# Kernel optimization log

Measured on AMD Instinct MI355X. Metric: run time of the kernel, lower is better.

## Reference

```python
import jax, jax.numpy as jnp
import numpy as np

N_NODES = 100_000
N_EDGES = 1_600_000
IN_DIM = 500
HID = 128
OUT = 16
DEG = 3          # Chebyshev 'order' -> DEG+1 basis terms
N_KAN_USED = 2   # forward applies kan_layers[:num_layers-1] with num_layers=3


def spmm(edge_index, h):
    # torch.sparse.mm(A, h) with A = COO(edge_index, ones, (N, N)):
    # out[row] = sum over edges of h[col]
    return jax.ops.segment_sum(h[edge_index[1]], edge_index[0], num_segments=N_NODES)


def cheb_kan(h, coeffs):
    # ChebyKANLayer: t = tanh(h); basis T_k(t) = cos(k*arccos(t)) computed via
    # the (mathematically identical, numerically stable) recurrence.
    t = jnp.tanh(h)                                  # [N, HID]
    Ts = [jnp.ones_like(t), t]
    for _ in range(DEG - 1):
        Ts.append(2.0 * t * Ts[-1] - Ts[-2])
    basis = jnp.stack(Ts, axis=-1)                   # [N, HID, DEG+1]
    return jnp.einsum('nid,iod->no', basis, coeffs)  # [N, HID]


def setup_inputs() -> dict:
    key = jax.random.key(0)
    ks = jax.random.split(key, 6)
    x = jax.random.normal(ks[0], (N_NODES, IN_DIM), dtype=jnp.float32)
    edge_index = jax.random.randint(ks[1], (2, N_EDGES), 0, N_NODES)
    W_in = jax.random.normal(ks[2], (IN_DIM, HID), dtype=jnp.float32) / np.sqrt(IN_DIM)
    cheb_coeffs = jax.random.normal(ks[3], (N_KAN_USED, HID, HID, DEG + 1),
                                    dtype=jnp.float32) / (HID * (DEG + 1))
    W_out = jax.random.normal(ks[4], (HID, OUT), dtype=jnp.float32) / np.sqrt(HID)
    return {"x": x, "edge_index": edge_index, "W_in": W_in,
            "cheb_coeffs": cheb_coeffs, "W_out": W_out}


def reference(x, edge_index, W_in, cheb_coeffs, W_out):
    h = x @ W_in                      # linear_input (no bias)
    # dropout is identity at inference
    h = spmm(edge_index, h)           # sparse adjacency aggregation
    for l in range(N_KAN_USED):
        h = cheb_kan(h, cheb_coeffs[l])
        h = spmm(edge_index, h)
    logits = h @ W_out                # output_layer (no bias)
    return jax.nn.log_softmax(logits, axis=-1)
```

## Files before the change

kernel.cpp:

```cpp
#include <hip/hip_runtime.h>
#include <hip/hip_bf16.h>

#define N_NODES 100000
#define N_EDGES 1600000
#define IN_DIM  500
#define HID     128
#define KDIM    512
#define NB      782
#define BCAP    4096

#define NG_GEMM 1563
#define NG_BIN  6250

typedef __attribute__((ext_vector_type(8))) short bf16x8;
typedef __attribute__((ext_vector_type(4))) float f32x4;

__device__ inline short f2bf(float x) {
    union { float f; unsigned u; } v; v.f = x;
    unsigned r = (v.u + 0x7FFFu + ((v.u >> 16) & 1u)) >> 16;
    return (short)r;
}
__device__ inline float bf_lo(unsigned u) { union { unsigned u; float f; } v; v.u = u << 16; return v.f; }
__device__ inline float bf_hi(unsigned u) { union { unsigned u; float f; } v; v.u = u & 0xFFFF0000u; return v.f; }

__device__ inline bf16x8 cheb_frag(unsigned v) {
    float hx[2] = {bf_lo(v), bf_hi(v)};
    short t[8];
#pragma unroll
    for (int q = 0; q < 2; q++) {
        float xx = fminf(fmaxf(hx[q], -15.f), 15.f);
        float e  = __expf(2.f * xx);
        float tt = (e - 1.f) / (e + 1.f);
        float T2 = 2.f * tt * tt - 1.f;
        float T3 = 2.f * tt * T2 - tt;
        t[q * 4 + 0] = (short)0x3F80;
        t[q * 4 + 1] = f2bf(tt);
        t[q * 4 + 2] = f2bf(T2);
        t[q * 4 + 3] = f2bf(T3);
    }
    return *(bf16x8*)&t[0];
}

__global__ __launch_bounds__(256) void repack_all(const float* __restrict__ cheb,
                                                  const float* __restrict__ W,
                                                  const float* __restrict__ Wout,
                                                  unsigned short* __restrict__ Bmat,
                                                  unsigned short* __restrict__ Wmat,
                                                  unsigned short* __restrict__ C2W) {
    const int b = blockIdx.x;
    if (b < 256) {
        int idx = b * 256 + threadIdx.x;
        int o = idx >> 9;
        int k = idx & 511;
        int i = k >> 2;
        int d = k & 3;
        Bmat[idx] = (unsigned short)f2bf(cheb[i * 512 + o * 4 + d]);
    } else if (b < 512) {
        int idx = (b - 256) * 256 + threadIdx.x;
        int o = idx >> 9;
        int k = idx & 511;
        Wmat[idx] = (k < IN_DIM) ? (unsigned short)f2bf(W[k * HID + o]) : 0;
    } else {
        int idx = (b - 512) * 256 + threadIdx.x;
        int o16 = idx >> 9;
        int k   = idx & 511;
        const float* cb = cheb + 65536 + (k >> 2) * 512 + (k & 3);
        float s = 0.f;
#pragma unroll 4
        for (int o = 0; o < 128; o++) s += cb[o * 4] * Wout[o * 16 + o16];
        C2W[o16 * 512 + k] = (unsigned short)f2bf(s);
    }
}

__global__ __launch_bounds__(256, 4) void prep_kernel(const float* __restrict__ x,
                                                      const int* __restrict__ ei,
                                                      const unsigned short* __restrict__ Wmat,
                                                      unsigned short* __restrict__ hA,
                                                      int* __restrict__ bcnt,
                                                      unsigned* __restrict__ bbuf) {
    __shared__ __align__(16) short Bs[2][128][40];
    const int tid = threadIdx.x;

    if (blockIdx.x < NG_GEMM) {
        const int lane = tid & 63;
        const int wave = tid >> 6;
        const int quad = lane >> 4;
        const int l16  = lane & 15;
        const int n0   = blockIdx.x * 64;
        const int br   = tid >> 1;
        const int bh   = tid & 1;

        int row = n0 + wave * 16 + l16; if (row >= N_NODES) row = N_NODES - 1;
        const float* __restrict__ xrow = x + (long)row * IN_DIM;

        f32x4 acc[8];
#pragma unroll
        for (int nt = 0; nt < 8; nt++)
#pragma unroll
            for (int r = 0; r < 4; r++) acc[nt][r] = 0.f;

        auto loadA = [&](int kt, float (&v)[8]) {
            const int kb = kt * 32 + quad * 8;
            if (kb + 8 <= IN_DIM) {
                const float4* s4 = (const float4*)(xrow + kb);
                float4 a0 = s4[0], a1 = s4[1];
                v[0]=a0.x; v[1]=a0.y; v[2]=a0.z; v[3]=a0.w;
                v[4]=a1.x; v[5]=a1.y; v[6]=a1.z; v[7]=a1.w;
            } else {
#pragma unroll
                for (int q = 0; q < 8; q++) v[q] = (kb + q < IN_DIM) ? xrow[kb + q] : 0.f;
            }
        };
        auto loadB = [&](int kt, bf16x8 (&w)[2]) {
            w[0] = *(const bf16x8*)&Wmat[br * 512 + kt * 32 + bh * 16];
            w[1] = *(const bf16x8*)&Wmat[br * 512 + kt * 32 + bh * 16 + 8];
        };
        auto storeB = [&](int buf, const bf16x8 (&w)[2]) {
            *(bf16x8*)&Bs[buf][br][bh * 16]     = w[0];
            *(bf16x8*)&Bs[buf][br][bh * 16 + 8] = w[1];
        };
        auto mfmaTile = [&](int buf, const float (&v)[8]) {
            short t[8];
#pragma unroll
            for (int q = 0; q < 8; q++) t[q] = f2bf(v[q]);
            bf16x8 a = *(bf16x8*)&t[0];
#pragma unroll
            for (int nt = 0; nt < 8; nt++) {
                bf16x8 b = *(const bf16x8*)&Bs[buf][nt * 16 + l16][quad * 8];
                acc[nt] = __builtin_amdgcn_mfma_f32_16x16x32_bf16(a, b, acc[nt], 0, 0, 0);
            }
        };

        float  va[8], vb[8];
        bf16x8 wa[2], wb[2];
        loadA(0, va); loadB(0, wa);
        for (int kt = 0; kt < 16; kt += 2) {
            storeB(0, wa);
            loadB(kt + 1, wb);
            loadA(kt + 1, vb);
            __syncthreads();
            mfmaTile(0, va);
            storeB(1, wb);
            if (kt + 2 < 16) { loadB(kt + 2, wa); loadA(kt + 2, va); }
            __syncthreads();
            mfmaTile(1, vb);
        }

        int mrow = n0 + wave * 16 + quad * 4;
#pragma unroll
        for (int r = 0; r < 4; r++) {
            int n = mrow + r;
            if (n < N_NODES) {
#pragma unroll
                for (int nt = 0; nt < 8; nt++)
                    hA[(long)n * HID + nt * 16 + l16] = (unsigned short)f2bf(acc[nt][r]);
            }
        }
    } else {
        int e = (blockIdx.x - NG_GEMM) * 256 + tid;
        if (e < N_EDGES) {
            int r = ei[e];
            int c = ei[N_EDGES + e];
            int b = r >> 7;
            int p = atomicAdd(&bcnt[b * 16], 1);
            if (p < BCAP) bbuf[b * BCAP + p] = ((unsigned)(r & 127) << 17) | (unsigned)c;
        }
    }
}

__global__ __launch_bounds__(256) void place_kernel(const unsigned* __restrict__ buf,
                                                    const int* __restrict__ bcnt,
                                                    int* __restrict__ gctr,
                                                    int* __restrict__ row_start,
                                                    int* __restrict__ row_cnt,
                                                    int* __restrict__ col_sorted) {
    __shared__ int hist[128];
    __shared__ int scan[128];
    __shared__ int cur[128];
    __shared__ int base_s;
    const int b = blockIdx.x, tid = threadIdx.x;
    int cnt = bcnt[b * 16]; if (cnt > BCAP) cnt = BCAP;
    if (tid < 128) hist[tid] = 0;
    __syncthreads();
    for (int i = tid; i < cnt; i += 256)
        atomicAdd(&hist[buf[b * BCAP + i] >> 17], 1);
    __syncthreads();
    if (tid < 128) scan[tid] = hist[tid];
    __syncthreads();
    for (int off = 1; off < 128; off <<= 1) {
        int t = (tid < 128 && tid >= off) ? scan[tid - off] : 0;
        __syncthreads();
        if (tid < 128) scan[tid] += t;
        __syncthreads();
    }
    if (tid == 0) base_s = atomicAdd(gctr, scan[127]);
    __syncthreads();
    const int base = base_s;
    if (tid < 128) {
        int excl = scan[tid] - hist[tid] + base;
        cur[tid] = excl;
        int r = b * 128 + tid;
        if (r < N_NODES) { row_start[r] = excl; row_cnt[r] = hist[tid]; }
    }
    __syncthreads();
    for (int i = tid; i < cnt; i += 256) {
        unsigned u = buf[b * BCAP + i];
        int rl = (int)(u >> 17);
        int c  = (int)(u & 0x1FFFFu);
        int pos = atomicAdd(&cur[rl], 1);
        col_sorted[pos] = c;
    }
}

__global__ __launch_bounds__(256, 4) void cheb_gemm(const unsigned short* __restrict__ h,
                                                    const unsigned short* __restrict__ Bmat,
                                                    unsigned short* __restrict__ out) {
    __shared__ __align__(16) short Bs[2][128][40];
    const int tid  = threadIdx.x;
    const int lane = tid & 63;
    const int wave = tid >> 6;
    const int quad = lane >> 4;
    const int l16  = lane & 15;
    const int n0   = blockIdx.x * 64;
    const int br   = tid >> 1;
    const int bh   = tid & 1;

    int row = n0 + wave * 16 + l16; if (row >= N_NODES) row = N_NODES - 1;
    const unsigned short* __restrict__ hrow = h + (long)row * HID;

    unsigned hreg[16];
#pragma unroll
    for (int kt = 0; kt < 16; kt++)
        hreg[kt] = *(const unsigned*)(hrow + kt * 8 + quad * 2);

    f32x4 acc[8];
#pragma unroll
    for (int nt = 0; nt < 8; nt++)
#pragma unroll
        for (int r = 0; r < 4; r++) acc[nt][r] = 0.f;

    auto loadB = [&](int kt, bf16x8 (&w)[2]) {
        w[0] = *(const bf16x8*)&Bmat[br * 512 + kt * 32 + bh * 16];
        w[1] = *(const bf16x8*)&Bmat[br * 512 + kt * 32 + bh * 16 + 8];
    };
    auto storeB = [&](int buf, const bf16x8 (&w)[2]) {
        *(bf16x8*)&Bs[buf][br][bh * 16]     = w[0];
        *(bf16x8*)&Bs[buf][br][bh * 16 + 8] = w[1];
    };
    auto mfmaTile = [&](int buf, int kt) {
        bf16x8 a = cheb_frag(hreg[kt]);
#pragma unroll
        for (int nt = 0; nt < 8; nt++) {
            bf16x8 b = *(const bf16x8*)&Bs[buf][nt * 16 + l16][quad * 8];
            acc[nt] = __builtin_amdgcn_mfma_f32_16x16x32_bf16(a, b, acc[nt], 0, 0, 0);
        }
    };

    bf16x8 wa[2], wb[2];
    loadB(0, wa);
    for (int kt = 0; kt < 16; kt += 2) {
        storeB(0, wa);
        loadB(kt + 1, wb);
        __syncthreads();
        mfmaTile(0, kt);
        storeB(1, wb);
        if (kt + 2 < 16) loadB(kt + 2, wa);
        __syncthreads();
        mfmaTile(1, kt + 1);
    }

    {
        int mrow = n0 + wave * 16 + quad * 4;
#pragma unroll
        for (int r = 0; r < 4; r++) {
            int n = mrow + r;
            if (n < N_NODES) {
#pragma unroll
                for (int nt = 0; nt < 8; nt++)
                    out[(long)n * HID + nt * 16 + l16] = (unsigned short)f2bf(acc[nt][r]);
            }
        }
    }
}

__global__ __launch_bounds__(256, 4) void cheb16_gemm(const unsigned short* __restrict__ h,
                                                      const unsigned short* __restrict__ C2W,
                                                      float* __restrict__ z) {
    __shared__ __align__(16) short Bs16[16][520];
    const int tid  = threadIdx.x;
    const int lane = tid & 63;
    const int wave = tid >> 6;
    const int quad = lane >> 4;
    const int l16  = lane & 15;
    const int n0   = blockIdx.x * 64;

    {
        int o16 = tid >> 4;
        int seg = tid & 15;
        *(bf16x8*)&Bs16[o16][seg * 32]      = *(const bf16x8*)&C2W[o16 * 512 + seg * 32];
        *(bf16x8*)&Bs16[o16][seg * 32 + 8]  = *(const bf16x8*)&C2W[o16 * 512 + seg * 32 + 8];
        *(bf16x8*)&Bs16[o16][seg * 32 + 16] = *(const bf16x8*)&C2W[o16 * 512 + seg * 32 + 16];
        *(bf16x8*)&Bs16[o16][seg * 32 + 24] = *(const bf16x8*)&C2W[o16 * 512 + seg * 32 + 24];
    }

    int row = n0 + wave * 16 + l16; if (row >= N_NODES) row = N_NODES - 1;
    const unsigned short* __restrict__ hrow = h + (long)row * HID;

    unsigned hreg[16];
#pragma unroll
    for (int kt = 0; kt < 16; kt++)
        hreg[kt] = *(const unsigned*)(hrow + kt * 8 + quad * 2);

    f32x4 acc;
#pragma unroll
    for (int r = 0; r < 4; r++) acc[r] = 0.f;

    __syncthreads();

#pragma unroll
    for (int kt = 0; kt < 16; kt++) {
        bf16x8 a = cheb_frag(hreg[kt]);
        bf16x8 b = *(const bf16x8*)&Bs16[l16][kt * 32 + quad * 8];
        acc = __builtin_amdgcn_mfma_f32_16x16x32_bf16(a, b, acc, 0, 0, 0);
    }

    {
        int mrow = n0 + wave * 16 + quad * 4;
#pragma unroll
        for (int r = 0; r < 4; r++) {
            int n = mrow + r;
            if (n < N_NODES) z[n * 16 + l16] = acc[r];
        }
    }
}

__global__ __launch_bounds__(256) void spmm_gather(const int* __restrict__ row_start,
                                                   const int* __restrict__ row_cnt,
                                                   const int* __restrict__ col_sorted,
                                                   const unsigned short* __restrict__ h,
                                                   unsigned short* __restrict__ out) {
    const int wid  = (blockIdx.x * 256 + threadIdx.x) >> 6;
    const int lane = threadIdx.x & 63;
    const int sub  = lane >> 4;
    const int fl   = lane & 15;
    if (wid >= N_NODES) return;
    const int s = row_start[wid];
    const int e = s + row_cnt[wid];
    const uint4* __restrict__ h4 = (const uint4*)h;

    float a[8], b[8];
#pragma unroll
    for (int q = 0; q < 8; q++) { a[q] = 0.f; b[q] = 0.f; }

    int j = s;
    for (; j + 8 <= e; j += 8) {
        int c0 = col_sorted[j + sub];
        int c1 = col_sorted[j + 4 + sub];
        uint4 u0 = h4[c0 * 16 + fl];
        uint4 u1 = h4[c1 * 16 + fl];
        a[0] += bf_lo(u0.x); a[1] += bf_hi(u0.x);
        a[2] += bf_lo(u0.y); a[3] += bf_hi(u0.y);
        a[4] += bf_lo(u0.z); a[5] += bf_hi(u0.z);
        a[6] += bf_lo(u0.w); a[7] += bf_hi(u0.w);
        b[0] += bf_lo(u1.x); b[1] += bf_hi(u1.x);
        b[2] += bf_lo(u1.y); b[3] += bf_hi(u1.y);
        b[4] += bf_lo(u1.z); b[5] += bf_hi(u1.z);
        b[6] += bf_lo(u1.w); b[7] += bf_hi(u1.w);
    }
    for (; j < e; j += 4) {
        int idx = j + sub;
        float m = (idx < e) ? 1.f : 0.f;
        int ci = (idx < e) ? idx : (e - 1);
        int c = col_sorted[ci];
        uint4 u = h4[c * 16 + fl];
        a[0] = fmaf(m, bf_lo(u.x), a[0]); a[1] = fmaf(m, bf_hi(u.x), a[1]);
        a[2] = fmaf(m, bf_lo(u.y), a[2]); a[3] = fmaf(m, bf_hi(u.y), a[3]);
        a[4] = fmaf(m, bf_lo(u.z), a[4]); a[5] = fmaf(m, bf_hi(u.z), a[5]);
        a[6] = fmaf(m, bf_lo(u.w), a[6]); a[7] = fmaf(m, bf_hi(u.w), a[7]);
    }
#pragma unroll
    for (int q = 0; q < 8; q++) a[q] += b[q];
#pragma unroll
    for (int q = 0; q < 8; q++) {
        a[q] += __shfl_xor(a[q], 16);
        a[q] += __shfl_xor(a[q], 32);
    }
    if (sub == 0) {
        unsigned w0 = (unsigned)(unsigned short)f2bf(a[0]) | ((unsigned)(unsigned short)f2bf(a[1]) << 16);
        unsigned w1 = (unsigned)(unsigned short)f2bf(a[2]) | ((unsigned)(unsigned short)f2bf(a[3]) << 16);
        unsigned w2 = (unsigned)(unsigned short)f2bf(a[4]) | ((unsigned)(unsigned short)f2bf(a[5]) << 16);
        unsigned w3 = (unsigned)(unsigned short)f2bf(a[6]) | ((unsigned)(unsigned short)f2bf(a[7]) << 16);
        uint4 pw; pw.x = w0; pw.y = w1; pw.z = w2; pw.w = w3;
        ((uint4*)out)[wid * 16 + fl] = pw;
    }
}

__global__ __launch_bounds__(256) void spmm_out(const int* __restrict__ row_start,
                                                const int* __restrict__ row_cnt,
                                                const int* __restrict__ col_sorted,
                                                const float* __restrict__ z,
                                                float* __restrict__ out) {
    const int wid  = (blockIdx.x * 256 + threadIdx.x) >> 6;
    const int lane = threadIdx.x & 63;
    const int sub  = lane >> 4;
    const int fl   = lane & 15;
    if (wid >= N_NODES) return;
    const int s = row_start[wid];
    const int e = s + row_cnt[wid];

    float a0 = 0.f, a1 = 0.f;
    int j = s;
    for (; j + 8 <= e; j += 8) {
        int c0 = col_sorted[j + sub];
        int c1 = col_sorted[j + 4 + sub];
        a0 += z[c0 * 16 + fl];
        a1 += z[c1 * 16 + fl];
    }
    for (; j < e; j += 4) {
        int idx = j + sub;
        float m = (idx < e) ? 1.f : 0.f;
        int ci = (idx < e) ? idx : (e - 1);
        a0 = fmaf(m, z[col_sorted[ci] * 16 + fl], a0);
    }
    float v = a0 + a1;
    v += __shfl_xor(v, 16);
    v += __shfl_xor(v, 32);
    float mx = v;
#pragma unroll
    for (int m = 8; m >= 1; m >>= 1) mx = fmaxf(mx, __shfl_xor(mx, m));
    float ex = expf(v - mx);
    float se = ex;
#pragma unroll
    for (int m = 8; m >= 1; m >>= 1) se += __shfl_xor(se, m);
    if (sub == 0) out[wid * 16 + fl] = v - mx - logf(se);
}


extern "C" void kernel_launch(void* const* d_in, const int* in_sizes, int n_in,
                              void* d_out, int out_size, void* d_ws, size_t ws_size,
                              hipStream_t stream) {
    const float* x     = (const float*)d_in[0];
    const int*   ei    = (const int*)d_in[1];
    const float* W_in  = (const float*)d_in[2];
    const float* cheb  = (const float*)d_in[3];
    const float* W_out = (const float*)d_in[4];
    float* out = (float*)d_out;

    char* p = (char*)d_ws;
    unsigned short* hA   = (unsigned short*)p; p += (size_t)N_NODES * HID * 2;
    unsigned short* hB   = (unsigned short*)p; p += (size_t)N_NODES * HID * 2;
    int*   col_sorted    = (int*)p;            p += (size_t)N_EDGES * 4;
    unsigned short* Bmat = (unsigned short*)p; p += (size_t)HID * KDIM * 2;
    unsigned short* Wmat = (unsigned short*)p; p += (size_t)HID * KDIM * 2;
    unsigned short* C2W  = (unsigned short*)p; p += (size_t)16 * KDIM * 2;
    float* zbuf          = (float*)p;          p += (size_t)N_NODES * 16 * 4;
    int*   row_start     = (int*)p;            p += (size_t)N_NODES * 4;
    int*   row_cnt       = (int*)p;            p += (size_t)N_NODES * 4;
    int*   bcnt          = (int*)p;            p += (size_t)(NB * 16 + 16) * 4;

    int* gctr = bcnt + NB * 16;

    unsigned* bbuf = (unsigned*)hB;

    const int nblk_prep = NG_GEMM + NG_BIN;
    const int nblk_gemm = (N_NODES + 63) / 64;
    const int nblk_spmm = (N_NODES + 3) / 4;

    hipMemsetAsync(bcnt, 0, (size_t)(NB * 16 + 16) * 4, stream);

    repack_all<<<544, 256, 0, stream>>>(cheb, W_in, W_out, Bmat, Wmat, C2W);

    prep_kernel<<<nblk_prep, 256, 0, stream>>>(x, ei, Wmat, hA, bcnt, bbuf);
    place_kernel<<<NB, 256, 0, stream>>>(bbuf, bcnt, gctr, row_start, row_cnt, col_sorted);

    spmm_gather<<<nblk_spmm, 256, 0, stream>>>(row_start, row_cnt, col_sorted, hA, hB);

    cheb_gemm<<<nblk_gemm, 256, 0, stream>>>(hB, Bmat, hA);
    spmm_gather<<<nblk_spmm, 256, 0, stream>>>(row_start, row_cnt, col_sorted, hA, hB);

    cheb16_gemm<<<nblk_gemm, 256, 0, stream>>>(hB, C2W, zbuf);
    spmm_out<<<nblk_spmm, 256, 0, stream>>>(row_start, row_cnt, col_sorted, zbuf, out);
}
```

Baseline: 626.0 us.

## Split edge binning from input GEMM and keep full W_in resident in LDS

Splits the fused prep kernel into a separate edge-binning kernel and a dedicated x@W_in GEMM. The new GEMM uses 512-thread blocks over 128 rows and loads the whole 128x512 bf16 weight matrix into LDS once, with an XOR swizzle against bank conflicts. This removes the per-k-tile double-buffered B staging and its barriers, and prefetches A two tiles ahead. In exchange it gives up overlap between binning and the GEMM inside one launch, and the 128 KB of LDS per block limits occupancy.

After: 648.4 us. 3.6% more time.

```diff
diff --git a/kernel.cpp b/kernel.cpp
--- a/kernel.cpp
+++ b/kernel.cpp
@@ -8,9 +8,6 @@
 #define KDIM    512
 #define NB      782
 #define BCAP    4096
-
-#define NG_GEMM 1563
-#define NG_BIN  6250
 
 typedef __attribute__((ext_vector_type(8))) short bf16x8;
 typedef __attribute__((ext_vector_type(4))) float f32x4;
@@ -39,6 +36,63 @@
         t[q * 4 + 3] = f2bf(T3);
     }
     return *(bf16x8*)&t[0];
+}
+
+__global__ __launch_bounds__(256) void bin_kernel(const int* __restrict__ ei,
+                                                  int* __restrict__ bcnt,
+                                                  unsigned* __restrict__ buf) {
+    int e = blockIdx.x * 256 + threadIdx.x;
+    if (e < N_EDGES) {
+        int r = ei[e];
+        int c = ei[N_EDGES + e];
+        int b = r >> 7;
+        int p = atomicAdd(&bcnt[b * 16], 1);
+        if (p < BCAP) buf[b * BCAP + p] = ((unsigned)(r & 127) << 17) | (unsigned)c;
+    }
+}
+
+__global__ __launch_bounds__(256) void place_kernel(const unsigned* __restrict__ buf,
+                                                    const int* __restrict__ bcnt,
+                                                    int* __restrict__ gctr,
+                                                    int* __restrict__ row_start,
+                                                    int* __restrict__ row_cnt,
+                                                    int* __restrict__ col_sorted) {
+    __shared__ int hist[128];
+    __shared__ int scan[128];
+    __shared__ int cur[128];
+    __shared__ int base_s;
+    const int b = blockIdx.x, tid = threadIdx.x;
+    int cnt = bcnt[b * 16]; if (cnt > BCAP) cnt = BCAP;
+    if (tid < 128) hist[tid] = 0;
+    __syncthreads();
+    for (int i = tid; i < cnt; i += 256)
+        atomicAdd(&hist[buf[b * BCAP + i] >> 17], 1);
+    __syncthreads();
+    if (tid < 128) scan[tid] = hist[tid];
+    __syncthreads();
+    for (int off = 1; off < 128; off <<= 1) {
+        int t = (tid < 128 && tid >= off) ? scan[tid - off] : 0;
+        __syncthreads();
+        if (tid < 128) scan[tid] += t;
+        __syncthreads();
+    }
+    if (tid == 0) base_s = atomicAdd(gctr, scan[127]);
+    __syncthreads();
+    const int base = base_s;
+    if (tid < 128) {
+        int excl = scan[tid] - hist[tid] + base;
+        cur[tid] = excl;
+        int r = b * 128 + tid;
+        if (r < N_NODES) { row_start[r] = excl; row_cnt[r] = hist[tid]; }
+    }
+    __syncthreads();
+    for (int i = tid; i < cnt; i += 256) {
+        unsigned u = buf[b * BCAP + i];
+        int rl = (int)(u >> 17);
+        int c  = (int)(u & 0x1FFFFu);
+        int pos = atomicAdd(&cur[rl], 1);
+        col_sorted[pos] = c;
+    }
 }
 
 __global__ __launch_bounds__(256) void repack_all(const float* __restrict__ cheb,
@@ -72,80 +126,72 @@
     }
 }
 
-__global__ __launch_bounds__(256, 4) void prep_kernel(const float* __restrict__ x,
-                                                      const int* __restrict__ ei,
-                                                      const unsigned short* __restrict__ Wmat,
-                                                      unsigned short* __restrict__ hA,
-                                                      int* __restrict__ bcnt,
-                                                      unsigned* __restrict__ bbuf) {
-    __shared__ __align__(16) short Bs[2][128][40];
-    const int tid = threadIdx.x;
-
-    if (blockIdx.x < NG_GEMM) {
-        const int lane = tid & 63;
-        const int wave = tid >> 6;
-        const int quad = lane >> 4;
-        const int l16  = lane & 15;
-        const int n0   = blockIdx.x * 64;
-        const int br   = tid >> 1;
-        const int bh   = tid & 1;
-
-        int row = n0 + wave * 16 + l16; if (row >= N_NODES) row = N_NODES - 1;
-        const float* __restrict__ xrow = x + (long)row * IN_DIM;
-
-        f32x4 acc[8];
-#pragma unroll
-        for (int nt = 0; nt < 8; nt++)
-#pragma unroll
-            for (int r = 0; r < 4; r++) acc[nt][r] = 0.f;
-
-        auto loadA = [&](int kt, float (&v)[8]) {
-            const int kb = kt * 32 + quad * 8;
-            if (kb + 8 <= IN_DIM) {
-                const float4* s4 = (const float4*)(xrow + kb);
-                float4 a0 = s4[0], a1 = s4[1];
-                v[0]=a0.x; v[1]=a0.y; v[2]=a0.z; v[3]=a0.w;
-                v[4]=a1.x; v[5]=a1.y; v[6]=a1.z; v[7]=a1.w;
-            } else {
-#pragma unroll
-                for (int q = 0; q < 8; q++) v[q] = (kb + q < IN_DIM) ? xrow[kb + q] : 0.f;
-            }
-        };
-        auto loadB = [&](int kt, bf16x8 (&w)[2]) {
-            w[0] = *(const bf16x8*)&Wmat[br * 512 + kt * 32 + bh * 16];
-            w[1] = *(const bf16x8*)&Wmat[br * 512 + kt * 32 + bh * 16 + 8];
-        };
-        auto storeB = [&](int buf, const bf16x8 (&w)[2]) {
-            *(bf16x8*)&Bs[buf][br][bh * 16]     = w[0];
-            *(bf16x8*)&Bs[buf][br][bh * 16 + 8] = w[1];
-        };
-        auto mfmaTile = [&](int buf, const float (&v)[8]) {
-            short t[8];
-#pragma unroll
-            for (int q = 0; q < 8; q++) t[q] = f2bf(v[q]);
-            bf16x8 a = *(bf16x8*)&t[0];
-#pragma unroll
-            for (int nt = 0; nt < 8; nt++) {
-                bf16x8 b = *(const bf16x8*)&Bs[buf][nt * 16 + l16][quad * 8];
-                acc[nt] = __builtin_amdgcn_mfma_f32_16x16x32_bf16(a, b, acc[nt], 0, 0, 0);
-            }
-        };
-
-        float  va[8], vb[8];
-        bf16x8 wa[2], wb[2];
-        loadA(0, va); loadB(0, wa);
-        for (int kt = 0; kt < 16; kt += 2) {
-            storeB(0, wa);
-            loadB(kt + 1, wb);
-            loadA(kt + 1, vb);
-            __syncthreads();
-            mfmaTile(0, va);
-            storeB(1, wb);
-            if (kt + 2 < 16) { loadB(kt + 2, wa); loadA(kt + 2, va); }
-            __syncthreads();
-            mfmaTile(1, vb);
-        }
-
+__global__ __launch_bounds__(512, 2) void gemm_xw(const float* __restrict__ x,
+                                                  const unsigned short* __restrict__ Wmat,
+                                                  unsigned short* __restrict__ out) {
+    __shared__ __align__(16) short Bs[128][512];
+    const int tid  = threadIdx.x;
+    const int lane = tid & 63;
+    const int wave = tid >> 6;
+    const int quad = lane >> 4;
+    const int l16  = lane & 15;
+    const int n0   = blockIdx.x * 128;
+
+    {
+        const int r  = tid >> 2;
+        const int s  = tid & 3;
+        const int xr = (r & 7) << 3;
+#pragma unroll
+        for (int i = 0; i < 16; i++) {
+            int c = s * 128 + i * 8;
+            *(bf16x8*)&Bs[r][c ^ xr] = *(const bf16x8*)&Wmat[r * 512 + c];
+        }
+    }
+
+    int row = n0 + wave * 16 + l16; if (row >= N_NODES) row = N_NODES - 1;
+    const float* __restrict__ xrow = x + (long)row * IN_DIM;
+    const int xrd = (l16 & 7) << 3;
+
+    f32x4 acc[8];
+#pragma unroll
+    for (int nt = 0; nt < 8; nt++)
+#pragma unroll
+        for (int r = 0; r < 4; r++) acc[nt][r] = 0.f;
+
+    auto loadA = [&](int kt, float (&v)[8]) {
+        const int kb = kt * 32 + quad * 8;
+        if (kb + 8 <= IN_DIM) {
+            const float4* s4 = (const float4*)(xrow + kb);
+            float4 a0 = s4[0], a1 = s4[1];
+            v[0]=a0.x; v[1]=a0.y; v[2]=a0.z; v[3]=a0.w;
+            v[4]=a1.x; v[5]=a1.y; v[6]=a1.z; v[7]=a1.w;
+        } else {
+#pragma unroll
+            for (int q = 0; q < 8; q++) v[q] = (kb + q < IN_DIM) ? xrow[kb + q] : 0.f;
+        }
+    };
+
+    float A[3][8];
+    loadA(0, A[0]);
+    loadA(1, A[1]);
+    __syncthreads();
+
+#pragma unroll
+    for (int kt = 0; kt < 16; kt++) {
+        if (kt + 2 < 16) loadA(kt + 2, A[(kt + 2) % 3]);
+        short t[8];
+#pragma unroll
+        for (int q = 0; q < 8; q++) t[q] = f2bf(A[kt % 3][q]);
+        bf16x8 a = *(bf16x8*)&t[0];
+        const int cb = kt * 32 + quad * 8;
+#pragma unroll
+        for (int nt = 0; nt < 8; nt++) {
+            bf16x8 b = *(const bf16x8*)&Bs[nt * 16 + l16][cb ^ xrd];
+            acc[nt] = __builtin_amdgcn_mfma_f32_16x16x32_bf16(a, b, acc[nt], 0, 0, 0);
+        }
+    }
+
+    {
         int mrow = n0 + wave * 16 + quad * 4;
 #pragma unroll
         for (int r = 0; r < 4; r++) {
@@ -153,62 +199,9 @@
             if (n < N_NODES) {
 #pragma unroll
                 for (int nt = 0; nt < 8; nt++)
-                    hA[(long)n * HID + nt * 16 + l16] = (unsigned short)f2bf(acc[nt][r]);
+                    out[(long)n * HID + nt * 16 + l16] = (unsigned short)f2bf(acc[nt][r]);
             }
         }
-    } else {
-        int e = (blockIdx.x - NG_GEMM) * 256 + tid;
-        if (e < N_EDGES) {
-            int r = ei[e];
-            int c = ei[N_EDGES + e];
-            int b = r >> 7;
-            int p = atomicAdd(&bcnt[b * 16], 1);
-            if (p < BCAP) bbuf[b * BCAP + p] = ((unsigned)(r & 127) << 17) | (unsigned)c;
-        }
-    }
-}
-
-__global__ __launch_bounds__(256) void place_kernel(const unsigned* __restrict__ buf,
-                                                    const int* __restrict__ bcnt,
-                                                    int* __restrict__ gctr,
-                                                    int* __restrict__ row_start,
-                                                    int* __restrict__ row_cnt,
-                                                    int* __restrict__ col_sorted) {
-    __shared__ int hist[128];
-    __shared__ int scan[128];
-    __shared__ int cur[128];
-    __shared__ int base_s;
-    const int b = blockIdx.x, tid = threadIdx.x;
-    int cnt = bcnt[b * 16]; if (cnt > BCAP) cnt = BCAP;
-    if (tid < 128) hist[tid] = 0;
-    __syncthreads();
-    for (int i = tid; i < cnt; i += 256)
-        atomicAdd(&hist[buf[b * BCAP + i] >> 17], 1);
-    __syncthreads();
-    if (tid < 128) scan[tid] = hist[tid];
-    __syncthreads();
-    for (int off = 1; off < 128; off <<= 1) {
-        int t = (tid < 128 && tid >= off) ? scan[tid - off] : 0;
-        __syncthreads();
-        if (tid < 128) scan[tid] += t;
-        __syncthreads();
-    }
-    if (tid == 0) base_s = atomicAdd(gctr, scan[127]);
-    __syncthreads();
-    const int base = base_s;
-    if (tid < 128) {
-        int excl = scan[tid] - hist[tid] + base;
-        cur[tid] = excl;
-        int r = b * 128 + tid;
-        if (r < N_NODES) { row_start[r] = excl; row_cnt[r] = hist[tid]; }
-    }
-    __syncthreads();
-    for (int i = tid; i < cnt; i += 256) {
-        unsigned u = buf[b * BCAP + i];
-        int rl = (int)(u >> 17);
-        int c  = (int)(u & 0x1FFFFu);
-        int pos = atomicAdd(&cur[rl], 1);
-        col_sorted[pos] = c;
     }
 }
 
@@ -462,16 +455,18 @@
 
     unsigned* bbuf = (unsigned*)hB;
 
-    const int nblk_prep = NG_GEMM + NG_BIN;
-    const int nblk_gemm = (N_NODES + 63) / 64;
-    const int nblk_spmm = (N_NODES + 3) / 4;
+    const int nblk_edge  = N_EDGES / 256;
+    const int nblk_gxw   = (N_NODES + 127) / 128;
+    const int nblk_gemm  = (N_NODES + 63) / 64;
+    const int nblk_spmm  = (N_NODES + 3) / 4;
 
     hipMemsetAsync(bcnt, 0, (size_t)(NB * 16 + 16) * 4, stream);
 
+    bin_kernel<<<nblk_edge, 256, 0, stream>>>(ei, bcnt, bbuf);
+    place_kernel<<<NB, 256, 0, stream>>>(bbuf, bcnt, gctr, row_start, row_cnt, col_sorted);
     repack_all<<<544, 256, 0, stream>>>(cheb, W_in, W_out, Bmat, Wmat, C2W);
 
-    prep_kernel<<<nblk_prep, 256, 0, stream>>>(x, ei, Wmat, hA, bcnt, bbuf);
-    place_kernel<<<NB, 256, 0, stream>>>(bbuf, bcnt, gctr, row_start, row_cnt, col_sorted);
+    gemm_xw<<<nblk_gxw, 512, 0, stream>>>(x, Wmat, hA);
 
     spmm_gather<<<nblk_spmm, 256, 0, stream>>>(row_start, row_cnt, col_sorted, hA, hB);
 
```

## Stage full x tile in swizzled LDS and read weights directly from global

Applied to the files above, without the earlier changes.

The input GEMM in prep_kernel now loads each block's full 64x500 slice of x once, with coalesced float4 loads per row. It converts the values to bf16 and stores them in a 64KB XOR-swizzled LDS tile. The B operand (Wmat) is no longer double-buffered through LDS; each MFMA reads it straight from global or L2, which removes per-k-tile syncthreads. The larger LDS footprint lowers launch bounds to 2 blocks per SIMD-group, trading occupancy and latency hiding for more coalesced x reads.

Result: slower. 693.9 us (+10.9%).

```diff
diff --git a/kernel.cpp b/kernel.cpp
--- a/kernel.cpp
+++ b/kernel.cpp
@@ -72,13 +72,13 @@
     }
 }
 
-__global__ __launch_bounds__(256, 4) void prep_kernel(const float* __restrict__ x,
+__global__ __launch_bounds__(256, 2) void prep_kernel(const float* __restrict__ x,
                                                       const int* __restrict__ ei,
                                                       const unsigned short* __restrict__ Wmat,
                                                       unsigned short* __restrict__ hA,
                                                       int* __restrict__ bcnt,
                                                       unsigned* __restrict__ bbuf) {
-    __shared__ __align__(16) short Bs[2][128][40];
+    __shared__ __align__(16) short As[64][512];
     const int tid = threadIdx.x;
 
     if (blockIdx.x < NG_GEMM) {
@@ -87,11 +87,24 @@
         const int quad = lane >> 4;
         const int l16  = lane & 15;
         const int n0   = blockIdx.x * 64;
-        const int br   = tid >> 1;
-        const int bh   = tid & 1;
-
-        int row = n0 + wave * 16 + l16; if (row >= N_NODES) row = N_NODES - 1;
-        const float* __restrict__ xrow = x + (long)row * IN_DIM;
+
+#pragma unroll
+        for (int r16 = 0; r16 < 16; r16++) {
+            const int slot = wave * 16 + r16;
+            int row = n0 + slot; if (row >= N_NODES) row = N_NODES - 1;
+            const float4* __restrict__ xr4 = (const float4*)(x + (long)row * IN_DIM);
+            const int xr = (r16 & 7) << 3;
+#pragma unroll
+            for (int i = 0; i < 2; i++) {
+                int idx = i * 64 + lane;
+                float4 v;
+                if (idx < 125) v = xr4[idx];
+                else { v.x = 0.f; v.y = 0.f; v.z = 0.f; v.w = 0.f; }
+                short t[4];
+                t[0] = f2bf(v.x); t[1] = f2bf(v.y); t[2] = f2bf(v.z); t[3] = f2bf(v.w);
+                *(unsigned long long*)&As[slot][(idx * 4) ^ xr] = *(unsigned long long*)&t[0];
+            }
+        }
 
         f32x4 acc[8];
 #pragma unroll
@@ -99,51 +112,18 @@
 #pragma unroll
             for (int r = 0; r < 4; r++) acc[nt][r] = 0.f;
 
-        auto loadA = [&](int kt, float (&v)[8]) {
-            const int kb = kt * 32 + quad * 8;
-            if (kb + 8 <= IN_DIM) {
-                const float4* s4 = (const float4*)(xrow + kb);
-                float4 a0 = s4[0], a1 = s4[1];
-                v[0]=a0.x; v[1]=a0.y; v[2]=a0.z; v[3]=a0.w;
-                v[4]=a1.x; v[5]=a1.y; v[6]=a1.z; v[7]=a1.w;
-            } else {
-#pragma unroll
-                for (int q = 0; q < 8; q++) v[q] = (kb + q < IN_DIM) ? xrow[kb + q] : 0.f;
-            }
-        };
-        auto loadB = [&](int kt, bf16x8 (&w)[2]) {
-            w[0] = *(const bf16x8*)&Wmat[br * 512 + kt * 32 + bh * 16];
-            w[1] = *(const bf16x8*)&Wmat[br * 512 + kt * 32 + bh * 16 + 8];
-        };
-        auto storeB = [&](int buf, const bf16x8 (&w)[2]) {
-            *(bf16x8*)&Bs[buf][br][bh * 16]     = w[0];
-            *(bf16x8*)&Bs[buf][br][bh * 16 + 8] = w[1];
-        };
-        auto mfmaTile = [&](int buf, const float (&v)[8]) {
-            short t[8];
-#pragma unroll
-            for (int q = 0; q < 8; q++) t[q] = f2bf(v[q]);
-            bf16x8 a = *(bf16x8*)&t[0];
+        __syncthreads();
+
+        const int arow = wave * 16 + l16;
+        const int axr  = (l16 & 7) << 3;
+#pragma unroll
+        for (int kt = 0; kt < 16; kt++) {
+            bf16x8 a = *(const bf16x8*)&As[arow][(kt * 32 + quad * 8) ^ axr];
 #pragma unroll
             for (int nt = 0; nt < 8; nt++) {
-                bf16x8 b = *(const bf16x8*)&Bs[buf][nt * 16 + l16][quad * 8];
+                bf16x8 b = *(const bf16x8*)&Wmat[(nt * 16 + l16) * 512 + kt * 32 + quad * 8];
                 acc[nt] = __builtin_amdgcn_mfma_f32_16x16x32_bf16(a, b, acc[nt], 0, 0, 0);
             }
-        };
-
-        float  va[8], vb[8];
-        bf16x8 wa[2], wb[2];
-        loadA(0, va); loadB(0, wa);
-        for (int kt = 0; kt < 16; kt += 2) {
-            storeB(0, wa);
-            loadB(kt + 1, wb);
-            loadA(kt + 1, vb);
-            __syncthreads();
-            mfmaTile(0, va);
-            storeB(1, wb);
-            if (kt + 2 < 16) { loadB(kt + 2, wa); loadA(kt + 2, va); }
-            __syncthreads();
-            mfmaTile(1, vb);
         }
 
         int mrow = n0 + wave * 16 + quad * 4;
```
